# Kernel optimization log

Hardware: AMD Instinct MI355X
Metric: run time of the kernel (lower is better)

Reference implementation:

```python
import jax, jax.numpy as jnp
import numpy as np

RADIUS = 9.0
GROUPS = 4
BLK = 64  # row block for streaming the N x N pairwise convolution


def leaky(x):
    return jnp.where(x >= 0, x, 0.2 * x)


def group_norm(x, gamma, beta, eps=1e-5):
    # x: (N, C); matches torch.nn.GroupNorm(GROUPS, C) applied to (1, C, N)
    N, C = x.shape
    xg = x.T.reshape(GROUPS, (C // GROUPS) * N)
    m = xg.mean(axis=1, keepdims=True)
    v = ((xg - m) ** 2).mean(axis=1, keepdims=True)
    xg = (xg - m) / jnp.sqrt(v + eps)
    return xg.reshape(C, N).T * gamma + beta


def tangent_vectors(n):
    # Duff et al. orthonormal tangent basis; n: (N,3) unit normals -> (N,2,3)
    x, y, z = n[:, 0], n[:, 1], n[:, 2]
    s = jnp.where(z >= 0, 1.0, -1.0)
    a = -1.0 / (s + z)
    b = x * y * a
    uv = jnp.stack([1 + s * x * x * a, s * b, -s * x, b, s + y * y * a, -y], axis=-1)
    return uv.reshape(-1, 2, 3)


def load_mesh(xyz, normals, weights):
    # Build oriented local frames nuv (N,3,3) as in dMaSIFConv_seg.load_mesh
    p = xyz / RADIUS
    uv = tangent_vectors(normals)                  # (N,2,3)
    diff = p[None, :, :] - p[:, None, :]           # (N,N,3): x_j - x_i
    d2 = jnp.sum(diff * diff, axis=-1)             # (N,N)
    cos = normals @ normals.T                      # (N,N)
    window = jnp.exp(-d2 * (2.0 - cos) ** 2)       # pseudo-geodesic Gaussian
    X = jnp.einsum('ikd,ijd->ijk', uv, diff)       # (N,N,2) tangent coords
    ov = jnp.einsum('ij,j,ijk->ik', window, weights[:, 0], X) + 1e-5  # (N,2)
    nrm = jnp.maximum(jnp.linalg.norm(ov, axis=-1, keepdims=True), 1e-12)
    ov = ov / nrm                                  # F.normalize
    ex, ey = ov[:, :1], ov[:, 1:]
    u, v = uv[:, 0, :], uv[:, 1, :]
    return jnp.stack([normals, ex * u + ey * v, -ey * u + ex * v], axis=1)


def dmasif_conv(points, nuv, feats,
                ni_w1, ni_b1, ni_w2, ni_b2, gn_in_g, gn_in_b,
                cv_a1, cv_b1, cv_a2, cv_b2,
                no_w1, no_b1, no_w2, no_b2, gn_out_g, gn_out_b):
    N = points.shape[0]
    H = ni_w1.shape[0]
    O = no_w1.shape[0]
    # net_in + GroupNorm
    h = leaky(feats @ ni_w1.T + ni_b1)
    h = leaky(h @ ni_w2.T + ni_b2)
    h = group_norm(h, gn_in_g, gn_in_b)            # (N,H)
    p = points / (np.sqrt(2.0) * RADIUS)
    n = jax.lax.stop_gradient(nuv[:, 0, :])        # normals detached in window

    p_blk = p.reshape(-1, BLK, 3)
    n_blk = n.reshape(-1, BLK, 3)
    nuv_blk = nuv.reshape(-1, BLK, 3, 3)

    @jax.checkpoint
    def step(carry, blk):
        pi, ni, nuvi = blk                                  # (B,3),(B,3),(B,3,3)
        diff = p[None, :, :] - pi[:, None, :]               # (B,N,3)
        d2 = jnp.sum(diff * diff, axis=-1)                  # (B,N)
        window = jnp.exp(-d2 * (2.0 - ni @ n.T) ** 2)       # (B,N)
        X = jnp.einsum('bkd,bnd->bnk', nuvi, diff)          # (B,N,3) local coords
        g = jax.nn.relu(jnp.einsum('bnk,ck->bnc', X, cv_a1) + cv_b1)  # (B,N,8)
        M = jax.nn.relu(jnp.einsum('bnc,fc->bnf', g, cv_a2) + cv_b2)  # (B,N,H*O)
        M = M.reshape(BLK, N, O, H)
        out = jnp.einsum('bn,bnoh,nh->bo', window, M, h)    # (B,O)
        return carry, out

    _, outs = jax.lax.scan(step, None, (p_blk, n_blk, nuv_blk))
    y = outs.reshape(N, O)
    y = leaky(y @ no_w1.T + no_b1)
    y = leaky(y @ no_w2.T + no_b2)
    return group_norm(y, gn_out_g, gn_out_b)


def setup_inputs() -> dict:
    key = jax.random.key(0)
    ks = jax.random.split(key, 32)
    N, I, U, H, O, C = 4096, 16, 16, 16, 16, 8
    nrm = jax.random.normal(ks[1], (N, 3), dtype=jnp.float32)
    nrm = nrm / jnp.linalg.norm(nrm, axis=-1, keepdims=True)
    w = lambda k, sh: 0.1 * jax.random.normal(k, sh, dtype=jnp.float32)
    return {
        'surface_xyz': 10.0 * jax.random.normal(ks[0], (N, 3), dtype=jnp.float32),
        'surface_normals': nrm,
        'features': jax.random.normal(ks[2], (N, I), dtype=jnp.float32),
        'os_w1': w(ks[3], (U, I)), 'os_b1': w(ks[4], (U,)),
        'os_w2': w(ks[5], (1, U)), 'os_b2': w(ks[6], (1,)),
        'ni_w1': w(ks[7], (H, I)), 'ni_b1': w(ks[8], (H,)),
        'ni_w2': w(ks[9], (H, H)), 'ni_b2': w(ks[10], (H,)),
        'gn_in_g': jnp.ones((H,), jnp.float32), 'gn_in_b': jnp.zeros((H,), jnp.float32),
        'cv_a1': w(ks[11], (C, 3)), 'cv_b1': w(ks[12], (C,)),
        'cv_a2': w(ks[13], (H * O, C)), 'cv_b2': w(ks[14], (H * O,)),
        'no_w1': w(ks[15], (O, H)), 'no_b1': w(ks[16], (O,)),
        'no_w2': w(ks[17], (O, O)), 'no_b2': w(ks[18], (O,)),
        'gn_out_g': jnp.ones((O,), jnp.float32), 'gn_out_b': jnp.zeros((O,), jnp.float32),
        'll_w1': w(ks[19], (O, O)), 'll_b1': w(ks[20], (O,)),
        'll_w2': w(ks[21], (O, O)), 'll_b2': w(ks[22], (O,)),
        'lt_w': w(ks[23], (O, I)), 'lt_b': w(ks[24], (O,)),
    }


def reference(surface_xyz, surface_normals, features,
              os_w1, os_b1, os_w2, os_b2,
              ni_w1, ni_b1, ni_w2, ni_b2, gn_in_g, gn_in_b,
              cv_a1, cv_b1, cv_a2, cv_b2,
              no_w1, no_b1, no_w2, no_b2, gn_out_g, gn_out_b,
              ll_w1, ll_b1, ll_w2, ll_b2, lt_w, lt_b):
    # orientation scores: Linear -> LeakyReLU(0.2) -> Linear
    scores = leaky(features @ os_w1.T + os_b1) @ os_w2.T + os_b2  # (N,1)
    nuv = load_mesh(surface_xyz, surface_normals, scores)
    # dMaSIFConv_seg forward, n_layers = 1
    x_i = dmasif_conv(surface_xyz, nuv, features,
                      ni_w1, ni_b1, ni_w2, ni_b2, gn_in_g, gn_in_b,
                      cv_a1, cv_b1, cv_a2, cv_b2,
                      no_w1, no_b1, no_w2, no_b2, gn_out_g, gn_out_b)
    x_i = jax.nn.relu(x_i @ ll_w1.T + ll_b1) @ ll_w2.T + ll_b2  # linear_layers[0]
    x = features @ lt_w.T + lt_b                                 # linear_transform[0]
    return x + x_i
```

## Files before the change

### kernel.cpp

```cpp
#include <hip/hip_runtime.h>

#define NP 4096
#define NJC 32
#define JCH (NP / NJC)
#define HR  12

typedef const float* fp;

using half4  = __attribute__((ext_vector_type(4))) __fp16;
using fp16x2 = __attribute__((ext_vector_type(2))) __fp16;
using f32x4  = __attribute__((ext_vector_type(4))) float;

__device__ __forceinline__ float lk(float x) { return x >= 0.f ? x : 0.2f * x; }

__device__ __forceinline__ unsigned int pkrtz(float a, float b) {
    fp16x2 h = __builtin_amdgcn_cvt_pkrtz(a, b);
    unsigned int u; __builtin_memcpy(&u, &h, 4); return u;
}
__device__ __forceinline__ fp16x2 u2h(unsigned int u) {
    fp16x2 h; __builtin_memcpy(&h, &u, 4); return h;
}
__device__ __forceinline__ fp16x2 pkmax0(fp16x2 a, fp16x2 z) {
    fp16x2 d;
    asm("v_pk_max_f16 %0, %1, %2" : "=v"(d) : "v"(a), "v"(z));
    return d;
}

#define OFF_CTR   0
#define OFF_PART1 4
#define OFF_PART2 132
#define OFF_OV    260
#define OFF_CONV  (260 + 2*NP)
#define OFF_SC    (260 + 18*NP)
#define OFF_UV    (OFF_SC  + NP)
#define OFF_P9    (OFF_UV  + 6*NP)
#define OFF_NRM   (OFF_P9  + 3*NP)
#define OFF_HPRE  (OFF_NRM + 3*NP)
#define OFF_NUV   (OFF_HPRE+ 16*NP)
#define WS_FLTS   (OFF_NUV + 9*NP)

__global__ __launch_bounds__(256) void k_prep(
    fp xyz, fp nrm, fp feats,
    fp osw1, fp osb1, fp osw2, fp osb2,
    fp niw1, fp nib1, fp niw2, fp nib2,
    float* __restrict__ ws)
{
    __shared__ float sR[4][8];
    const int tid = threadIdx.x;
    const int i = blockIdx.x * 256 + tid;
    const int wv = tid >> 6;

    ws[OFF_OV + i * 2]     = 0.f;
    ws[OFF_OV + i * 2 + 1] = 0.f;
    {
        float4 z4 = make_float4(0.f, 0.f, 0.f, 0.f);
        float4* c4 = (float4*)(ws + OFF_CONV + i * 16);
        c4[0] = z4; c4[1] = z4; c4[2] = z4; c4[3] = z4;
    }
    if (blockIdx.x == 0 && tid == 0) *(unsigned*)(ws + OFF_CTR) = 0u;

    float f[16];
#pragma unroll
    for (int c = 0; c < 16; c++) f[c] = feats[i * 16 + c];

    float sc = osb2[0];
#pragma unroll
    for (int u = 0; u < 16; u++) {
        float a = osb1[u];
#pragma unroll
        for (int c = 0; c < 16; c++) a += osw1[u * 16 + c] * f[c];
        sc += osw2[u] * lk(a);
    }
    ws[OFF_SC + i] = sc;

    float h1[16];
#pragma unroll
    for (int u = 0; u < 16; u++) {
        float a = nib1[u];
#pragma unroll
        for (int c = 0; c < 16; c++) a += niw1[u * 16 + c] * f[c];
        h1[u] = lk(a);
    }
    float h2[16];
#pragma unroll
    for (int u = 0; u < 16; u++) {
        float a = nib2[u];
#pragma unroll
        for (int c = 0; c < 16; c++) a += niw2[u * 16 + c] * h1[c];
        h2[u] = lk(a);
        ws[OFF_HPRE + i * 16 + u] = h2[u];
    }

#pragma unroll
    for (int g = 0; g < 4; g++) {
        float s = 0.f, ss = 0.f;
#pragma unroll
        for (int k = 0; k < 4; k++) { float v = h2[g * 4 + k]; s += v; ss += v * v; }
#pragma unroll
        for (int off = 32; off > 0; off >>= 1) {
            s  += __shfl_down(s,  off);
            ss += __shfl_down(ss, off);
        }
        if ((tid & 63) == 0) { sR[wv][g] = s; sR[wv][4 + g] = ss; }
    }
    __syncthreads();
    if (tid < 8) {
        float v = sR[0][tid] + sR[1][tid] + sR[2][tid] + sR[3][tid];
        ws[OFF_PART1 + blockIdx.x * 8 + tid] = v;
    }

    float nx = nrm[i * 3], ny = nrm[i * 3 + 1], nz = nrm[i * 3 + 2];
    float s  = (nz >= 0.f) ? 1.f : -1.f;
    float a  = -1.f / (s + nz);
    float b  = nx * ny * a;
    float ux = 1.f + s * nx * nx * a, uy = s * b,            uz = -s * nx;
    float vx = b,                     vy = s + ny * ny * a,  vz = -ny;
    ws[OFF_UV + i * 6 + 0] = ux; ws[OFF_UV + i * 6 + 1] = uy; ws[OFF_UV + i * 6 + 2] = uz;
    ws[OFF_UV + i * 6 + 3] = vx; ws[OFF_UV + i * 6 + 4] = vy; ws[OFF_UV + i * 6 + 5] = vz;
    const float IR = 1.f / 9.f;
    ws[OFF_P9 + i * 3 + 0] = xyz[i * 3 + 0] * IR;
    ws[OFF_P9 + i * 3 + 1] = xyz[i * 3 + 1] * IR;
    ws[OFF_P9 + i * 3 + 2] = xyz[i * 3 + 2] * IR;
    ws[OFF_NRM + i * 3 + 0] = nx;
    ws[OFF_NRM + i * 3 + 1] = ny;
    ws[OFF_NRM + i * 3 + 2] = nz;
}

__global__ __launch_bounds__(256) void k_mesh(float* __restrict__ ws)
{
    __shared__ float sp[3][512];
    __shared__ float sn[3][512];
    __shared__ float ssc[512];
    __shared__ float red[256][2];

    const int tid = threadIdx.x;
    const int ib = blockIdx.x >> 3, jc = blockIdx.x & 7;
    const int il = tid & 63, sub = tid >> 6;
    const int i = ib * 64 + il;
    const int j0 = jc * 512;

    for (int t = tid; t < 512; t += 256) {
        int j = j0 + t;
        sp[0][t] = ws[OFF_P9 + j * 3];     sp[1][t] = ws[OFF_P9 + j * 3 + 1];  sp[2][t] = ws[OFF_P9 + j * 3 + 2];
        sn[0][t] = ws[OFF_NRM + j * 3];    sn[1][t] = ws[OFF_NRM + j * 3 + 1]; sn[2][t] = ws[OFF_NRM + j * 3 + 2];
        ssc[t]   = ws[OFF_SC + j];
    }
    __syncthreads();

    const float pix = ws[OFF_P9 + i * 3], piy = ws[OFF_P9 + i * 3 + 1], piz = ws[OFF_P9 + i * 3 + 2];
    const float nix = ws[OFF_NRM + i * 3], niy = ws[OFF_NRM + i * 3 + 1], niz = ws[OFF_NRM + i * 3 + 2];
    const float ux = ws[OFF_UV + i * 6],     uy = ws[OFF_UV + i * 6 + 1], uz = ws[OFF_UV + i * 6 + 2];
    const float vx = ws[OFF_UV + i * 6 + 3], vy = ws[OFF_UV + i * 6 + 4], vz = ws[OFF_UV + i * 6 + 5];

    float ov0 = 0.f, ov1 = 0.f;
#pragma unroll 4
    for (int t = 0; t < 128; t++) {
        int j = sub * 128 + t;
        float dx = sp[0][j] - pix, dy = sp[1][j] - piy, dz = sp[2][j] - piz;
        float d2 = dx * dx + dy * dy + dz * dz;
        float cs = nix * sn[0][j] + niy * sn[1][j] + niz * sn[2][j];
        float tt = 2.f - cs;
        float w  = __expf(-d2 * tt * tt) * ssc[j];
        ov0 += w * (ux * dx + uy * dy + uz * dz);
        ov1 += w * (vx * dx + vy * dy + vz * dz);
    }
    red[tid][0] = ov0; red[tid][1] = ov1;
    __syncthreads();
    if (sub == 0) {
        float a = ov0 + red[64 + il][0] + red[128 + il][0] + red[192 + il][0];
        float b = ov1 + red[64 + il][1] + red[128 + il][1] + red[192 + il][1];
        atomicAdd(&ws[OFF_OV + i * 2],     a);
        atomicAdd(&ws[OFF_OV + i * 2 + 1], b);
    }
}

__global__ __launch_bounds__(256, 4) void k_conv(
    float* __restrict__ ws,
    const float* __restrict__ cva1, const float* __restrict__ cvb1,
    const float* __restrict__ A2,   const float* __restrict__ B2,
    fp gng, fp gnb,
    float* __restrict__ conv)
{
    __shared__ float4 sP[JCH];
    __shared__ float4 sN[JCH];
    __shared__ __align__(16) unsigned int sH2[JCH * HR];
    __shared__ float sGN[8];

    const int tid  = threadIdx.x;
    const int ib   = blockIdx.x >> 5;
    const int jc   = blockIdx.x & 31;
    const int j0   = jc * JCH;
    const int lane = tid & 63;
    const int wv   = tid >> 6;
    const int o    = lane & 15;
    const int quad = lane >> 4;
    const float IVS2 = 0.70710678118654752f;

    if (tid < 4) {
        float s = 0.f, q = 0.f;
#pragma unroll
        for (int b = 0; b < 16; b++) {
            s += ws[OFF_PART1 + b * 8 + tid];
            q += ws[OFF_PART1 + b * 8 + 4 + tid];
        }
        const float invM = 1.f / (4.f * NP);
        float m   = s * invM;
        float var = q * invM - m * m;
        sGN[tid]     = m;
        sGN[4 + tid] = rsqrtf(var + 1e-5f);
    }
    if (tid < 64) {
        const int ii = ib * 64 + tid;
        float o0 = ws[OFF_OV + ii * 2]     + 1e-5f;
        float o1 = ws[OFF_OV + ii * 2 + 1] + 1e-5f;
        float rnr = rsqrtf(fmaxf(o0 * o0 + o1 * o1, 1e-24f));
        float ex = o0 * rnr, ey = o1 * rnr;
        float uxx = ws[OFF_UV + ii * 6],     uyy = ws[OFF_UV + ii * 6 + 1], uzz = ws[OFF_UV + ii * 6 + 2];
        float vxx = ws[OFF_UV + ii * 6 + 3], vyy = ws[OFF_UV + ii * 6 + 4], vzz = ws[OFF_UV + ii * 6 + 5];
        ws[OFF_NUV + ii * 9 + 0] = ws[OFF_NRM + ii * 3];
        ws[OFF_NUV + ii * 9 + 1] = ws[OFF_NRM + ii * 3 + 1];
        ws[OFF_NUV + ii * 9 + 2] = ws[OFF_NRM + ii * 3 + 2];
        ws[OFF_NUV + ii * 9 + 3] =  ex * uxx + ey * vxx;
        ws[OFF_NUV + ii * 9 + 4] =  ex * uyy + ey * vyy;
        ws[OFF_NUV + ii * 9 + 5] =  ex * uzz + ey * vzz;
        ws[OFF_NUV + ii * 9 + 6] = -ey * uxx + ex * vxx;
        ws[OFF_NUV + ii * 9 + 7] = -ey * uyy + ex * vyy;
        ws[OFF_NUV + ii * 9 + 8] = -ey * uzz + ex * vzz;
    }
    __syncthreads();

    if (tid < JCH) {
        const int t = tid;
        const int j = j0 + t;
        sP[t] = make_float4(ws[OFF_P9 + j * 3] * IVS2,
                            ws[OFF_P9 + j * 3 + 1] * IVS2,
                            ws[OFF_P9 + j * 3 + 2] * IVS2, 0.f);
        sN[t] = make_float4(ws[OFF_NRM + j * 3],
                            ws[OFF_NRM + j * 3 + 1],
                            ws[OFF_NRM + j * 3 + 2], 0.f);
        const float4* hs = (const float4*)(ws + OFF_HPRE + j * 16);
        float4 h0 = hs[0], h1 = hs[1], h2 = hs[2], h3 = hs[3];
        const float4* gg4 = (const float4*)gng;
        const float4* gb4 = (const float4*)gnb;
        float4 ga0 = gg4[0], ga1 = gg4[1], ga2 = gg4[2], ga3 = gg4[3];
        float4 gb0 = gb4[0], gb1 = gb4[1], gb2 = gb4[2], gb3 = gb4[3];
        const float m0 = sGN[0], m1 = sGN[1], m2 = sGN[2], m3 = sGN[3];
        const float v0 = sGN[4], v1 = sGN[5], v2 = sGN[6], v3 = sGN[7];
        h0.x = (h0.x - m0) * v0 * ga0.x + gb0.x; h0.y = (h0.y - m0) * v0 * ga0.y + gb0.y;
        h0.z = (h0.z - m0) * v0 * ga0.z + gb0.z; h0.w = (h0.w - m0) * v0 * ga0.w + gb0.w;
        h1.x = (h1.x - m1) * v1 * ga1.x + gb1.x; h1.y = (h1.y - m1) * v1 * ga1.y + gb1.y;
        h1.z = (h1.z - m1) * v1 * ga1.z + gb1.z; h1.w = (h1.w - m1) * v1 * ga1.w + gb1.w;
        h2.x = (h2.x - m2) * v2 * ga2.x + gb2.x; h2.y = (h2.y - m2) * v2 * ga2.y + gb2.y;
        h2.z = (h2.z - m2) * v2 * ga2.z + gb2.z; h2.w = (h2.w - m2) * v2 * ga2.w + gb2.w;
        h3.x = (h3.x - m3) * v3 * ga3.x + gb3.x; h3.y = (h3.y - m3) * v3 * ga3.y + gb3.y;
        h3.z = (h3.z - m3) * v3 * ga3.z + gb3.z; h3.w = (h3.w - m3) * v3 * ga3.w + gb3.w;
        uint4 w0, w1;
        w0.x = pkrtz(h0.x, h0.y); w0.y = pkrtz(h0.z, h0.w);
        w0.z = pkrtz(h1.x, h1.y); w0.w = pkrtz(h1.z, h1.w);
        w1.x = pkrtz(h2.x, h2.y); w1.y = pkrtz(h2.z, h2.w);
        w1.z = pkrtz(h3.x, h3.y); w1.w = pkrtz(h3.z, h3.w);
        *(uint4*)(sH2 + t * HR)     = w0;
        *(uint4*)(sH2 + t * HR + 4) = w1;
    }

    half4 Bf[16];
#pragma unroll
    for (int t = 0; t < 16; t++) {
        half4 v = {(__fp16)0.f, (__fp16)0.f, (__fp16)0.f, (__fp16)0.f};
        const float* row = A2 + (o * 16 + t) * 8;
        if (quad == 0) {
#pragma unroll
            for (int c = 0; c < 4; c++) v[c] = (__fp16)row[c];
        } else if (quad == 1) {
#pragma unroll
            for (int c = 0; c < 4; c++) v[c] = (__fp16)row[4 + c];
        } else if (quad == 2) {
            v[0] = (__fp16)B2[o * 16 + t];
        }
        Bf[t] = v;
    }

    float a1[24], b1c[8];
#pragma unroll
    for (int k = 0; k < 24; k++) a1[k] = cva1[k];
#pragma unroll
    for (int k = 0; k < 8; k++)  b1c[k] = cvb1[k];

    __syncthreads();

    const f32x4 zc = {0.f, 0.f, 0.f, 0.f};
    const fp16x2 h2z = {(__fp16)0.f, (__fp16)0.f};
    const int o4 = o << 2;

#pragma unroll 1
    for (int ii = 0; ii < 16; ii++) {
        const int i = ib * 64 + wv * 16 + ii;
        const float pix = ws[OFF_P9 + i * 3 + 0] * IVS2;
        const float piy = ws[OFF_P9 + i * 3 + 1] * IVS2;
        const float piz = ws[OFF_P9 + i * 3 + 2] * IVS2;
        float r[9];
#pragma unroll
        for (int k = 0; k < 9; k++) r[k] = ws[OFF_NUV + i * 9 + k];

        float accO = 0.f;

#pragma unroll 1
        for (int jg = 0; jg < JCH / 64; jg++) {
            const int jl = jg * 64 + lane;
            const float4 pj = sP[jl];
            const float4 nj = sN[jl];
            const float dx = pj.x - pix, dy = pj.y - piy, dz = pj.z - piz;
            const float d2 = dx * dx + dy * dy + dz * dz;
            const float cs = r[0] * nj.x + r[1] * nj.y + r[2] * nj.z;
            const float tt = 2.f - cs;
            const float wwin = __expf(-d2 * tt * tt);
            const float X0 = r[0] * dx + r[1] * dy + r[2] * dz;
            const float X1 = r[3] * dx + r[4] * dy + r[5] * dz;
            const float X2 = r[6] * dx + r[7] * dy + r[8] * dz;
            float g[8];
#pragma unroll
            for (int c = 0; c < 8; c++)
                g[c] = fmaxf(a1[c * 3] * X0 + a1[c * 3 + 1] * X1 +
                             a1[c * 3 + 2] * X2 + b1c[c], 0.f);
            const int wg0 = (int)pkrtz(wwin * g[0], wwin * g[1]);
            const int wg1 = (int)pkrtz(wwin * g[2], wwin * g[3]);
            const int wg2 = (int)pkrtz(wwin * g[4], wwin * g[5]);
            const int wg3 = (int)pkrtz(wwin * g[6], wwin * g[7]);
            const int whp = (int)pkrtz(wwin, 0.f);

#pragma unroll 1
            for (int tau = 0; tau < 4; tau++) {
                const int srcb = tau * 64 + o4;
                const unsigned u0 = (unsigned)__builtin_amdgcn_ds_bpermute(srcb, wg0);
                const unsigned u1 = (unsigned)__builtin_amdgcn_ds_bpermute(srcb, wg1);
                const unsigned u2 = (unsigned)__builtin_amdgcn_ds_bpermute(srcb, wg2);
                const unsigned u3 = (unsigned)__builtin_amdgcn_ds_bpermute(srcb, wg3);
                const unsigned uw = (unsigned)__builtin_amdgcn_ds_bpermute(srcb, whp);
                uint2 av;
                av.x = (quad == 0) ? u0 : (quad == 1) ? u2 : (quad == 2) ? uw : 0u;
                av.y = (quad == 0) ? u1 : (quad == 1) ? u3 : 0u;
                half4 Af; __builtin_memcpy(&Af, &av, 8);

#pragma unroll
                for (int hq = 0; hq < 2; hq++) {
                    fp16x2 P[16];
#pragma unroll
                    for (int q2 = 0; q2 < 4; q2++) {
                        const int q = hq * 4 + q2;
                        f32x4 C0 = __builtin_amdgcn_mfma_f32_16x16x16f16(Af, Bf[2 * q],     zc, 0, 0, 0);
                        f32x4 C1 = __builtin_amdgcn_mfma_f32_16x16x16f16(Af, Bf[2 * q + 1], zc, 0, 0, 0);
#pragma unroll
                        for (int r2 = 0; r2 < 4; r2++) {
                            fp16x2 pp = __builtin_amdgcn_cvt_pkrtz(C0[r2], C1[r2]);
                            P[r2 * 4 + q2] = pkmax0(pp, h2z);
                        }
                    }
#pragma unroll
                    for (int r2 = 0; r2 < 4; r2++) {
                        const unsigned int* hr =
                            sH2 + (jg * 64 + tau * 16 + quad * 4 + r2) * HR + hq * 4;
                        const uint4 ha = *(const uint4*)hr;
                        accO = __builtin_amdgcn_fdot2(P[r2 * 4 + 0], u2h(ha.x), accO, false);
                        accO = __builtin_amdgcn_fdot2(P[r2 * 4 + 1], u2h(ha.y), accO, false);
                        accO = __builtin_amdgcn_fdot2(P[r2 * 4 + 2], u2h(ha.z), accO, false);
                        accO = __builtin_amdgcn_fdot2(P[r2 * 4 + 3], u2h(ha.w), accO, false);
                    }
                }
            }
        }

        accO += __shfl_xor(accO, 16, 64);
        accO += __shfl_xor(accO, 32, 64);
        if (lane < 16) atomicAdd(&conv[i * 16 + o], accO);
    }
}

__global__ __launch_bounds__(256) void k_post(
    float* __restrict__ ws, fp feats,
    fp now1, fp nob1, fp now2, fp nob2,
    fp gg, fp gb,
    fp llw1, fp llb1, fp llw2, fp llb2, fp ltw, fp ltb,
    float* __restrict__ out)
{
    __shared__ float sR[4][8];
    __shared__ float sP2[128];
    const int tid = threadIdx.x;
    const int i = blockIdx.x * 256 + tid;
    const int wv = tid >> 6;

    float cv[16];
#pragma unroll
    for (int o = 0; o < 16; o++) cv[o] = ws[OFF_CONV + i * 16 + o];

    float y1[16];
#pragma unroll
    for (int u = 0; u < 16; u++) {
        float a = nob1[u];
#pragma unroll
        for (int k = 0; k < 16; k++) a += now1[u * 16 + k] * cv[k];
        y1[u] = lk(a);
    }
    float y2[16];
#pragma unroll
    for (int u = 0; u < 16; u++) {
        float a = nob2[u];
#pragma unroll
        for (int k = 0; k < 16; k++) a += now2[u * 16 + k] * y1[k];
        y2[u] = lk(a);
    }

#pragma unroll
    for (int g = 0; g < 4; g++) {
        float s = 0.f, ss = 0.f;
#pragma unroll
        for (int k = 0; k < 4; k++) { float v = y2[g * 4 + k]; s += v; ss += v * v; }
#pragma unroll
        for (int off = 32; off > 0; off >>= 1) {
            s  += __shfl_down(s,  off);
            ss += __shfl_down(ss, off);
        }
        if ((tid & 63) == 0) { sR[wv][g] = s; sR[wv][4 + g] = ss; }
    }
    __syncthreads();
    if (tid < 8) {
        float v = sR[0][tid] + sR[1][tid] + sR[2][tid] + sR[3][tid];
        __hip_atomic_store(&ws[OFF_PART2 + blockIdx.x * 8 + tid], v,
                           __ATOMIC_RELEASE, __HIP_MEMORY_SCOPE_AGENT);
    }
    __syncthreads();

    unsigned* ctr = (unsigned*)(ws + OFF_CTR);
    if (tid == 0) {
        __hip_atomic_fetch_add(ctr, 1u, __ATOMIC_ACQ_REL, __HIP_MEMORY_SCOPE_AGENT);
        while (__hip_atomic_load(ctr, __ATOMIC_ACQUIRE, __HIP_MEMORY_SCOPE_AGENT) < gridDim.x)
            __builtin_amdgcn_s_sleep(8);
    }
    __syncthreads();

    if (tid < 128)
        sP2[tid] = __hip_atomic_load(&ws[OFF_PART2 + tid],
                                     __ATOMIC_ACQUIRE, __HIP_MEMORY_SCOPE_AGENT);
    __syncthreads();

    const float invM = 1.f / (4.f * NP);
    float z[16];
#pragma unroll
    for (int c = 0; c < 16; c++) {
        int g = c >> 2;
        float s = 0.f, q = 0.f;
#pragma unroll
        for (int b = 0; b < 16; b++) { s += sP2[b * 8 + g]; q += sP2[b * 8 + 4 + g]; }
        float m   = s * invM;
        float var = q * invM - m * m;
        float inv = rsqrtf(var + 1e-5f);
        z[c] = (y2[c] - m) * inv * gg[c] + gb[c];
    }
    float r1[16];
#pragma unroll
    for (int o = 0; o < 16; o++) {
        float a = llb1[o];
#pragma unroll
        for (int k = 0; k < 16; k++) a += llw1[o * 16 + k] * z[k];
        r1[o] = fmaxf(a, 0.f);
    }
    float f[16];
#pragma unroll
    for (int c = 0; c < 16; c++) f[c] = feats[i * 16 + c];
#pragma unroll
    for (int o = 0; o < 16; o++) {
        float a = llb2[o];
#pragma unroll
        for (int k = 0; k < 16; k++) a += llw2[o * 16 + k] * r1[k];
        float x = ltb[o];
#pragma unroll
        for (int k = 0; k < 16; k++) x += ltw[o * 16 + k] * f[k];
        out[i * 16 + o] = x + a;
    }
}

extern "C" void kernel_launch(void* const* d_in, const int* in_sizes, int n_in,
                              void* d_out, int out_size, void* d_ws, size_t ws_size,
                              hipStream_t stream)
{
    fp xyz  = (fp)d_in[0];
    fp nrm  = (fp)d_in[1];
    fp fts  = (fp)d_in[2];
    fp osw1 = (fp)d_in[3],  osb1 = (fp)d_in[4],  osw2 = (fp)d_in[5],  osb2 = (fp)d_in[6];
    fp niw1 = (fp)d_in[7],  nib1 = (fp)d_in[8],  niw2 = (fp)d_in[9],  nib2 = (fp)d_in[10];
    fp gng  = (fp)d_in[11], gnb  = (fp)d_in[12];
    fp cva1 = (fp)d_in[13], cvb1 = (fp)d_in[14], cva2 = (fp)d_in[15], cvb2 = (fp)d_in[16];
    fp now1 = (fp)d_in[17], nob1 = (fp)d_in[18], now2 = (fp)d_in[19], nob2 = (fp)d_in[20];
    fp gog  = (fp)d_in[21], gob  = (fp)d_in[22];
    fp llw1 = (fp)d_in[23], llb1 = (fp)d_in[24], llw2 = (fp)d_in[25], llb2 = (fp)d_in[26];
    fp ltw  = (fp)d_in[27], ltb  = (fp)d_in[28];

    float* ws = (float*)d_ws;

    k_prep<<<NP / 256, 256, 0, stream>>>(xyz, nrm, fts,
                                         osw1, osb1, osw2, osb2,
                                         niw1, nib1, niw2, nib2, ws);
    k_mesh<<<512, 256, 0, stream>>>(ws);
    k_conv<<<64 * NJC, 256, 0, stream>>>(ws, cva1, cvb1, cva2, cvb2,
                                         gng, gnb, ws + OFF_CONV);
    k_post<<<NP / 256, 256, 0, stream>>>(ws, fts, now1, nob1, now2, nob2,
                                         gog, gob, llw1, llb1, llw2, llb2,
                                         ltw, ltb, (float*)d_out);
}
```

Baseline: 459.0 us.

## Fold prep kernel into mesh kernel and replace atomics with per-chunk partials

Removes the separate k_prep launch. k_mesh now recomputes orientation scores and tangent frames from the raw inputs, and its jc==0 blocks write the per-point data, the net_in MLP output and the GroupNorm partials. The atomicAdd accumulation of orientation vectors is replaced by per-chunk partial buffers that k_conv sums. k_conv keeps the nuv frames in shared memory instead of writing them to global memory and reading them back. In exchange, the score MLP is recomputed redundantly across the 64 row blocks, and the jc==0 blocks carry extra serial work.

```diff
diff --git a/kernel.cpp b/kernel.cpp
--- a/kernel.cpp
+++ b/kernel.cpp
@@ -28,106 +28,21 @@
 
 #define OFF_CTR   0
 #define OFF_PART1 4
-#define OFF_PART2 132
-#define OFF_OV    260
-#define OFF_CONV  (260 + 2*NP)
-#define OFF_SC    (260 + 18*NP)
-#define OFF_UV    (OFF_SC  + NP)
+#define OFF_PART2 516
+#define OFF_OVP   644
+#define OFF_CONV  (644 + 16*NP)
+#define OFF_UV    (644 + 32*NP)
 #define OFF_P9    (OFF_UV  + 6*NP)
 #define OFF_NRM   (OFF_P9  + 3*NP)
 #define OFF_HPRE  (OFF_NRM + 3*NP)
-#define OFF_NUV   (OFF_HPRE+ 16*NP)
-#define WS_FLTS   (OFF_NUV + 9*NP)
-
-__global__ __launch_bounds__(256) void k_prep(
+#define WS_FLTS   (OFF_HPRE + 16*NP)
+
+__global__ __launch_bounds__(256) void k_mesh(
     fp xyz, fp nrm, fp feats,
     fp osw1, fp osb1, fp osw2, fp osb2,
     fp niw1, fp nib1, fp niw2, fp nib2,
     float* __restrict__ ws)
 {
-    __shared__ float sR[4][8];
-    const int tid = threadIdx.x;
-    const int i = blockIdx.x * 256 + tid;
-    const int wv = tid >> 6;
-
-    ws[OFF_OV + i * 2]     = 0.f;
-    ws[OFF_OV + i * 2 + 1] = 0.f;
-    {
-        float4 z4 = make_float4(0.f, 0.f, 0.f, 0.f);
-        float4* c4 = (float4*)(ws + OFF_CONV + i * 16);
-        c4[0] = z4; c4[1] = z4; c4[2] = z4; c4[3] = z4;
-    }
-    if (blockIdx.x == 0 && tid == 0) *(unsigned*)(ws + OFF_CTR) = 0u;
-
-    float f[16];
-#pragma unroll
-    for (int c = 0; c < 16; c++) f[c] = feats[i * 16 + c];
-
-    float sc = osb2[0];
-#pragma unroll
-    for (int u = 0; u < 16; u++) {
-        float a = osb1[u];
-#pragma unroll
-        for (int c = 0; c < 16; c++) a += osw1[u * 16 + c] * f[c];
-        sc += osw2[u] * lk(a);
-    }
-    ws[OFF_SC + i] = sc;
-
-    float h1[16];
-#pragma unroll
-    for (int u = 0; u < 16; u++) {
-        float a = nib1[u];
-#pragma unroll
-        for (int c = 0; c < 16; c++) a += niw1[u * 16 + c] * f[c];
-        h1[u] = lk(a);
-    }
-    float h2[16];
-#pragma unroll
-    for (int u = 0; u < 16; u++) {
-        float a = nib2[u];
-#pragma unroll
-        for (int c = 0; c < 16; c++) a += niw2[u * 16 + c] * h1[c];
-        h2[u] = lk(a);
-        ws[OFF_HPRE + i * 16 + u] = h2[u];
-    }
-
-#pragma unroll
-    for (int g = 0; g < 4; g++) {
-        float s = 0.f, ss = 0.f;
-#pragma unroll
-        for (int k = 0; k < 4; k++) { float v = h2[g * 4 + k]; s += v; ss += v * v; }
-#pragma unroll
-        for (int off = 32; off > 0; off >>= 1) {
-            s  += __shfl_down(s,  off);
-            ss += __shfl_down(ss, off);
-        }
-        if ((tid & 63) == 0) { sR[wv][g] = s; sR[wv][4 + g] = ss; }
-    }
-    __syncthreads();
-    if (tid < 8) {
-        float v = sR[0][tid] + sR[1][tid] + sR[2][tid] + sR[3][tid];
-        ws[OFF_PART1 + blockIdx.x * 8 + tid] = v;
-    }
-
-    float nx = nrm[i * 3], ny = nrm[i * 3 + 1], nz = nrm[i * 3 + 2];
-    float s  = (nz >= 0.f) ? 1.f : -1.f;
-    float a  = -1.f / (s + nz);
-    float b  = nx * ny * a;
-    float ux = 1.f + s * nx * nx * a, uy = s * b,            uz = -s * nx;
-    float vx = b,                     vy = s + ny * ny * a,  vz = -ny;
-    ws[OFF_UV + i * 6 + 0] = ux; ws[OFF_UV + i * 6 + 1] = uy; ws[OFF_UV + i * 6 + 2] = uz;
-    ws[OFF_UV + i * 6 + 3] = vx; ws[OFF_UV + i * 6 + 4] = vy; ws[OFF_UV + i * 6 + 5] = vz;
-    const float IR = 1.f / 9.f;
-    ws[OFF_P9 + i * 3 + 0] = xyz[i * 3 + 0] * IR;
-    ws[OFF_P9 + i * 3 + 1] = xyz[i * 3 + 1] * IR;
-    ws[OFF_P9 + i * 3 + 2] = xyz[i * 3 + 2] * IR;
-    ws[OFF_NRM + i * 3 + 0] = nx;
-    ws[OFF_NRM + i * 3 + 1] = ny;
-    ws[OFF_NRM + i * 3 + 2] = nz;
-}
-
-__global__ __launch_bounds__(256) void k_mesh(float* __restrict__ ws)
-{
     __shared__ float sp[3][512];
     __shared__ float sn[3][512];
     __shared__ float ssc[512];
@@ -138,19 +53,38 @@
     const int il = tid & 63, sub = tid >> 6;
     const int i = ib * 64 + il;
     const int j0 = jc * 512;
+    const float IR = 1.f / 9.f;
 
     for (int t = tid; t < 512; t += 256) {
         int j = j0 + t;
-        sp[0][t] = ws[OFF_P9 + j * 3];     sp[1][t] = ws[OFF_P9 + j * 3 + 1];  sp[2][t] = ws[OFF_P9 + j * 3 + 2];
-        sn[0][t] = ws[OFF_NRM + j * 3];    sn[1][t] = ws[OFF_NRM + j * 3 + 1]; sn[2][t] = ws[OFF_NRM + j * 3 + 2];
-        ssc[t]   = ws[OFF_SC + j];
-    }
-    __syncthreads();
-
-    const float pix = ws[OFF_P9 + i * 3], piy = ws[OFF_P9 + i * 3 + 1], piz = ws[OFF_P9 + i * 3 + 2];
-    const float nix = ws[OFF_NRM + i * 3], niy = ws[OFF_NRM + i * 3 + 1], niz = ws[OFF_NRM + i * 3 + 2];
-    const float ux = ws[OFF_UV + i * 6],     uy = ws[OFF_UV + i * 6 + 1], uz = ws[OFF_UV + i * 6 + 2];
-    const float vx = ws[OFF_UV + i * 6 + 3], vy = ws[OFF_UV + i * 6 + 4], vz = ws[OFF_UV + i * 6 + 5];
+        sp[0][t] = xyz[j * 3] * IR;
+        sp[1][t] = xyz[j * 3 + 1] * IR;
+        sp[2][t] = xyz[j * 3 + 2] * IR;
+        sn[0][t] = nrm[j * 3];
+        sn[1][t] = nrm[j * 3 + 1];
+        sn[2][t] = nrm[j * 3 + 2];
+        float fj[16];
+#pragma unroll
+        for (int c = 0; c < 16; c++) fj[c] = feats[j * 16 + c];
+        float sc = osb2[0];
+#pragma unroll
+        for (int u = 0; u < 16; u++) {
+            float a = osb1[u];
+#pragma unroll
+            for (int c = 0; c < 16; c++) a += osw1[u * 16 + c] * fj[c];
+            sc += osw2[u] * lk(a);
+        }
+        ssc[t] = sc;
+    }
+    __syncthreads();
+
+    const float pix = xyz[i * 3] * IR, piy = xyz[i * 3 + 1] * IR, piz = xyz[i * 3 + 2] * IR;
+    const float nix = nrm[i * 3], niy = nrm[i * 3 + 1], niz = nrm[i * 3 + 2];
+    const float sgn = (niz >= 0.f) ? 1.f : -1.f;
+    const float aa  = -1.f / (sgn + niz);
+    const float bb  = nix * niy * aa;
+    const float ux = 1.f + sgn * nix * nix * aa, uy = sgn * bb,            uz = -sgn * nix;
+    const float vx = bb,                         vy = sgn + niy * niy * aa, vz = -niy;
 
     float ov0 = 0.f, ov1 = 0.f;
 #pragma unroll 4
@@ -169,8 +103,59 @@
     if (sub == 0) {
         float a = ov0 + red[64 + il][0] + red[128 + il][0] + red[192 + il][0];
         float b = ov1 + red[64 + il][1] + red[128 + il][1] + red[192 + il][1];
-        atomicAdd(&ws[OFF_OV + i * 2],     a);
-        atomicAdd(&ws[OFF_OV + i * 2 + 1], b);
+        ws[OFF_OVP + jc * 2 * NP + i * 2]     = a;
+        ws[OFF_OVP + jc * 2 * NP + i * 2 + 1] = b;
+    }
+
+    if (jc == 0) {
+        ((float4*)(ws + OFF_CONV))[ib * 256 + tid] = make_float4(0.f, 0.f, 0.f, 0.f);
+        if (ib == 0 && tid == 0) *(unsigned*)(ws + OFF_CTR) = 0u;
+        if (tid < 64) {
+            ws[OFF_P9 + i * 3 + 0] = pix;
+            ws[OFF_P9 + i * 3 + 1] = piy;
+            ws[OFF_P9 + i * 3 + 2] = piz;
+            ws[OFF_NRM + i * 3 + 0] = nix;
+            ws[OFF_NRM + i * 3 + 1] = niy;
+            ws[OFF_NRM + i * 3 + 2] = niz;
+            ws[OFF_UV + i * 6 + 0] = ux; ws[OFF_UV + i * 6 + 1] = uy; ws[OFF_UV + i * 6 + 2] = uz;
+            ws[OFF_UV + i * 6 + 3] = vx; ws[OFF_UV + i * 6 + 4] = vy; ws[OFF_UV + i * 6 + 5] = vz;
+
+            float fi[16];
+#pragma unroll
+            for (int c = 0; c < 16; c++) fi[c] = feats[i * 16 + c];
+            float h1[16];
+#pragma unroll
+            for (int u = 0; u < 16; u++) {
+                float a = nib1[u];
+#pragma unroll
+                for (int c = 0; c < 16; c++) a += niw1[u * 16 + c] * fi[c];
+                h1[u] = lk(a);
+            }
+            float h2[16];
+#pragma unroll
+            for (int u = 0; u < 16; u++) {
+                float a = nib2[u];
+#pragma unroll
+                for (int c = 0; c < 16; c++) a += niw2[u * 16 + c] * h1[c];
+                h2[u] = lk(a);
+                ws[OFF_HPRE + i * 16 + u] = h2[u];
+            }
+#pragma unroll
+            for (int g = 0; g < 4; g++) {
+                float s = 0.f, ss = 0.f;
+#pragma unroll
+                for (int k = 0; k < 4; k++) { float v = h2[g * 4 + k]; s += v; ss += v * v; }
+#pragma unroll
+                for (int off = 32; off > 0; off >>= 1) {
+                    s  += __shfl_down(s,  off);
+                    ss += __shfl_down(ss, off);
+                }
+                if (tid == 0) {
+                    ws[OFF_PART1 + ib * 8 + g]     = s;
+                    ws[OFF_PART1 + ib * 8 + 4 + g] = ss;
+                }
+            }
+        }
     }
 }
 
@@ -185,6 +170,7 @@
     __shared__ float4 sN[JCH];
     __shared__ __align__(16) unsigned int sH2[JCH * HR];
     __shared__ float sGN[8];
+    __shared__ float sNUV[64][9];
 
     const int tid  = threadIdx.x;
     const int ib   = blockIdx.x >> 5;
@@ -199,7 +185,7 @@
     if (tid < 4) {
         float s = 0.f, q = 0.f;
 #pragma unroll
-        for (int b = 0; b < 16; b++) {
+        for (int b = 0; b < 64; b++) {
             s += ws[OFF_PART1 + b * 8 + tid];
             q += ws[OFF_PART1 + b * 8 + 4 + tid];
         }
@@ -211,21 +197,26 @@
     }
     if (tid < 64) {
         const int ii = ib * 64 + tid;
-        float o0 = ws[OFF_OV + ii * 2]     + 1e-5f;
-        float o1 = ws[OFF_OV + ii * 2 + 1] + 1e-5f;
+        float o0 = 0.f, o1 = 0.f;
+#pragma unroll
+        for (int c = 0; c < 8; c++) {
+            o0 += ws[OFF_OVP + c * 2 * NP + ii * 2];
+            o1 += ws[OFF_OVP + c * 2 * NP + ii * 2 + 1];
+        }
+        o0 += 1e-5f; o1 += 1e-5f;
         float rnr = rsqrtf(fmaxf(o0 * o0 + o1 * o1, 1e-24f));
         float ex = o0 * rnr, ey = o1 * rnr;
         float uxx = ws[OFF_UV + ii * 6],     uyy = ws[OFF_UV + ii * 6 + 1], uzz = ws[OFF_UV + ii * 6 + 2];
         float vxx = ws[OFF_UV + ii * 6 + 3], vyy = ws[OFF_UV + ii * 6 + 4], vzz = ws[OFF_UV + ii * 6 + 5];
-        ws[OFF_NUV + ii * 9 + 0] = ws[OFF_NRM + ii * 3];
-        ws[OFF_NUV + ii * 9 + 1] = ws[OFF_NRM + ii * 3 + 1];
-        ws[OFF_NUV + ii * 9 + 2] = ws[OFF_NRM + ii * 3 + 2];
-        ws[OFF_NUV + ii * 9 + 3] =  ex * uxx + ey * vxx;
-        ws[OFF_NUV + ii * 9 + 4] =  ex * uyy + ey * vyy;
-        ws[OFF_NUV + ii * 9 + 5] =  ex * uzz + ey * vzz;
-        ws[OFF_NUV + ii * 9 + 6] = -ey * uxx + ex * vxx;
-        ws[OFF_NUV + ii * 9 + 7] = -ey * uyy + ex * vyy;
-        ws[OFF_NUV + ii * 9 + 8] = -ey * uzz + ex * vzz;
+        sNUV[tid][0] = ws[OFF_NRM + ii * 3];
+        sNUV[tid][1] = ws[OFF_NRM + ii * 3 + 1];
+        sNUV[tid][2] = ws[OFF_NRM + ii * 3 + 2];
+        sNUV[tid][3] =  ex * uxx + ey * vxx;
+        sNUV[tid][4] =  ex * uyy + ey * vyy;
+        sNUV[tid][5] =  ex * uzz + ey * vzz;
+        sNUV[tid][6] = -ey * uxx + ex * vxx;
+        sNUV[tid][7] = -ey * uyy + ex * vyy;
+        sNUV[tid][8] = -ey * uzz + ex * vzz;
     }
     __syncthreads();
 
@@ -300,7 +291,7 @@
         const float piz = ws[OFF_P9 + i * 3 + 2] * IVS2;
         float r[9];
 #pragma unroll
-        for (int k = 0; k < 9; k++) r[k] = ws[OFF_NUV + i * 9 + k];
+        for (int k = 0; k < 9; k++) r[k] = sNUV[wv * 16 + ii][k];
 
         float accO = 0.f;
 
@@ -496,10 +487,9 @@
 
     float* ws = (float*)d_ws;
 
-    k_prep<<<NP / 256, 256, 0, stream>>>(xyz, nrm, fts,
-                                         osw1, osb1, osw2, osb2,
-                                         niw1, nib1, niw2, nib2, ws);
-    k_mesh<<<512, 256, 0, stream>>>(ws);
+    k_mesh<<<512, 256, 0, stream>>>(xyz, nrm, fts,
+                                    osw1, osb1, osw2, osb2,
+                                    niw1, nib1, niw2, nib2, ws);
     k_conv<<<64 * NJC, 256, 0, stream>>>(ws, cva1, cvb1, cva2, cvb2,
                                          gng, gnb, ws + OFF_CONV);
     k_post<<<NP / 256, 256, 0, stream>>>(ws, fts, now1, nob1, now2, nob2,
```

Measured after the change: 466.2 us. About the same (+1.6%).
